# Kernel optimization log

Measured on AMD Instinct MI355X. Metric: run time of the kernel, lower is better.

Reference implementation:

```python
import jax, jax.numpy as jnp
import numpy as np


def setup_inputs() -> dict:
    key = jax.random.key(0)
    k1, k2 = jax.random.split(key)
    N1, N2 = 16384, 16384
    pos1 = jax.random.normal(k1, (N1, 2), dtype=jnp.float32)
    pos2 = jax.random.normal(k2, (N2, 2), dtype=jnp.float32)
    return {"pos1": pos1, "pos2": pos2}


def reference(pos1, pos2):
    # pos1: [N1, 2], pos2: [N2, 2]
    diff = pos1[:, None, :] - pos2[None, :, :]          # [N1, N2, 2]
    dist = jnp.sqrt(jnp.sum(diff * diff, axis=2))       # [N1, N2]
    nearest = jnp.min(dist, axis=1)                     # [N1]
    return jnp.mean(nearest)
```

## Files before the change

kernel.cpp:

```cpp
#include <hip/hip_runtime.h>
#include <math.h>

#define N1 16384
#define N2 16384
#define BLOCK 256
#define PTS 8
#define I_BLOCKS (N1 / (BLOCK * PTS))
#define SLICES 128

__device__ __forceinline__ unsigned int f2key(float f) {
    unsigned int b = __float_as_uint(f);
    return (b & 0x80000000u) ? ~b : (b | 0x80000000u);
}
__device__ __forceinline__ float key2f(unsigned int k) {
    unsigned int b = (k & 0x80000000u) ? (k & 0x7FFFFFFFu) : ~k;
    return __uint_as_float(b);
}

__global__ __launch_bounds__(BLOCK, 4)
void nn_partial(const float2* __restrict__ pos1,
                const float4* __restrict__ pos2,
                unsigned int* __restrict__ keys,
                unsigned int* __restrict__ ticket,
                int slice_f4) {
    const int ib = blockIdx.x;
    const int sl = blockIdx.y;
    const int t  = threadIdx.x;

    if (ib == 0 && sl == 0 && t == 0) *ticket = 0;

    const float4* __restrict__ q = pos2 + (size_t)sl * slice_f4;
    const int i0 = ib * (BLOCK * PTS) + t;

    float x[PTS], y[PTS], m[PTS];
#pragma unroll
    for (int k = 0; k < PTS; ++k) {
        float2 p = pos1[i0 + k * BLOCK];
        x[k] = p.x; y[k] = p.y; m[k] = 3.4e38f;
    }

#pragma unroll 4
    for (int j = 0; j < slice_f4; ++j) {
        float4 qq = q[j];
        float ax = -2.f * qq.x, ay = -2.f * qq.y;
        float az = fmaf(qq.x, qq.x, qq.y * qq.y);
        float bx = -2.f * qq.z, by = -2.f * qq.w;
        float bz = fmaf(qq.z, qq.z, qq.w * qq.w);
#pragma unroll
        for (int k = 0; k < PTS; ++k) {
            m[k] = fminf(m[k], fmaf(x[k], ax, fmaf(y[k], ay, az)));
            m[k] = fminf(m[k], fmaf(x[k], bx, fmaf(y[k], by, bz)));
        }
    }

#pragma unroll
    for (int k = 0; k < PTS; ++k) {
        atomicMin(&keys[i0 + k * BLOCK], f2key(m[k]));
    }
}

__global__ __launch_bounds__(BLOCK)
void nn_finish(const unsigned int* __restrict__ keys,
               const float2* __restrict__ pos1,
               float* __restrict__ blocksums,
               unsigned int* __restrict__ ticket,
               float* __restrict__ out) {
    const int t = threadIdx.x;
    const int i = blockIdx.x * BLOCK + t;

    float g = key2f(keys[i]);
    float2 p = pos1[i];
    float d2 = fmaxf(fmaf(p.x, p.x, p.y * p.y) + g, 0.f);
    float sum = sqrtf(d2);

    for (int off = 32; off > 0; off >>= 1) {
        sum += __shfl_down(sum, off, 64);
    }
    __shared__ float wsum[BLOCK / 64];
    __shared__ int lastflag;
    if ((t & 63) == 0) wsum[t >> 6] = sum;
    __syncthreads();
    if (t == 0) {
        float s = 0.f;
        for (int w = 0; w < BLOCK / 64; ++w) s += wsum[w];
        blocksums[blockIdx.x] = s;
        __threadfence();
        unsigned int old = atomicAdd(ticket, 1u);
        lastflag = (old == gridDim.x - 1) ? 1 : 0;
    }
    __syncthreads();
    if (lastflag && t < 64) {
        volatile float* vb = (volatile float*)blocksums;
        float v = vb[t];
        for (int off = 32; off > 0; off >>= 1) {
            v += __shfl_down(v, off, 64);
        }
        if (t == 0) out[0] = v / (float)N1;
    }
}

extern "C" void kernel_launch(void* const* d_in, const int* in_sizes, int n_in,
                              void* d_out, int out_size, void* d_ws, size_t ws_size,
                              hipStream_t stream) {
    const float2* pos1 = (const float2*)d_in[0];
    const float4* pos2 = (const float4*)d_in[1];
    float* out = (float*)d_out;

    unsigned int* keys = (unsigned int*)d_ws;
    float* blocksums   = (float*)(keys + N1);
    unsigned int* ticket = (unsigned int*)(blocksums + 64);

    const int slice_f4 = (N2 / SLICES) / 2;

    hipMemsetAsync(keys, 0xFF, (size_t)N1 * sizeof(unsigned int), stream);

    dim3 grid1(I_BLOCKS, SLICES);
    nn_partial<<<grid1, BLOCK, 0, stream>>>(pos1, pos2, keys, ticket, slice_f4);
    nn_finish<<<N1 / BLOCK, BLOCK, 0, stream>>>(keys, pos1, blocksums, ticket, out);
}
```

Baseline: 78.07 us.

## Pack FMAs into 2-wide vectors and replace atomicMin with per-slice partials

The inner distance loop now uses 2-wide float vectors so the compiler can emit packed FMA instructions, and the -2 scaling moves onto the pos1 coordinates so it is done once per point instead of per pos2 element. The atomicMin on order-preserving keys and the memset are replaced by plain stores of per-slice minima into an N1×SLICES workspace, which the finish kernel reduces. This removes the atomics and the memset launch, but adds an 8 MB write and read of partials and a 128-iteration serial loop per thread in the finish kernel. The fminf calls stay scalar.

```diff
diff --git a/kernel.cpp b/kernel.cpp
--- a/kernel.cpp
+++ b/kernel.cpp
@@ -5,22 +5,16 @@
 #define N2 16384
 #define BLOCK 256
 #define PTS 8
+#define KK (PTS / 2)
 #define I_BLOCKS (N1 / (BLOCK * PTS))
 #define SLICES 128
 
-__device__ __forceinline__ unsigned int f2key(float f) {
-    unsigned int b = __float_as_uint(f);
-    return (b & 0x80000000u) ? ~b : (b | 0x80000000u);
-}
-__device__ __forceinline__ float key2f(unsigned int k) {
-    unsigned int b = (k & 0x80000000u) ? (k & 0x7FFFFFFFu) : ~k;
-    return __uint_as_float(b);
-}
+typedef float v2f __attribute__((ext_vector_type(2)));
 
 __global__ __launch_bounds__(BLOCK, 4)
 void nn_partial(const float2* __restrict__ pos1,
                 const float4* __restrict__ pos2,
-                unsigned int* __restrict__ keys,
+                float* __restrict__ partials,
                 unsigned int* __restrict__ ticket,
                 int slice_f4) {
     const int ib = blockIdx.x;
@@ -32,35 +26,44 @@
     const float4* __restrict__ q = pos2 + (size_t)sl * slice_f4;
     const int i0 = ib * (BLOCK * PTS) + t;
 
-    float x[PTS], y[PTS], m[PTS];
+    v2f x2[KK], y2[KK], m2[KK];
 #pragma unroll
-    for (int k = 0; k < PTS; ++k) {
-        float2 p = pos1[i0 + k * BLOCK];
-        x[k] = p.x; y[k] = p.y; m[k] = 3.4e38f;
+    for (int k = 0; k < KK; ++k) {
+        float2 p0 = pos1[i0 + (2 * k) * BLOCK];
+        float2 p1 = pos1[i0 + (2 * k + 1) * BLOCK];
+        x2[k] = (v2f){-2.f * p0.x, -2.f * p1.x};
+        y2[k] = (v2f){-2.f * p0.y, -2.f * p1.y};
+        m2[k] = (v2f){3.4e38f, 3.4e38f};
     }
 
 #pragma unroll 4
     for (int j = 0; j < slice_f4; ++j) {
         float4 qq = q[j];
-        float ax = -2.f * qq.x, ay = -2.f * qq.y;
         float az = fmaf(qq.x, qq.x, qq.y * qq.y);
-        float bx = -2.f * qq.z, by = -2.f * qq.w;
         float bz = fmaf(qq.z, qq.z, qq.w * qq.w);
+        v2f AX = {qq.x, qq.x}, AY = {qq.y, qq.y}, AZ = {az, az};
+        v2f BX = {qq.z, qq.z}, BY = {qq.w, qq.w}, BZ = {bz, bz};
 #pragma unroll
-        for (int k = 0; k < PTS; ++k) {
-            m[k] = fminf(m[k], fmaf(x[k], ax, fmaf(y[k], ay, az)));
-            m[k] = fminf(m[k], fmaf(x[k], bx, fmaf(y[k], by, bz)));
+        for (int k = 0; k < KK; ++k) {
+            v2f ta = __builtin_elementwise_fma(
+                x2[k], AX, __builtin_elementwise_fma(y2[k], AY, AZ));
+            v2f tb = __builtin_elementwise_fma(
+                x2[k], BX, __builtin_elementwise_fma(y2[k], BY, BZ));
+            m2[k][0] = fminf(m2[k][0], fminf(ta[0], tb[0]));
+            m2[k][1] = fminf(m2[k][1], fminf(ta[1], tb[1]));
         }
     }
 
+    float* dst = partials + (size_t)sl * N1 + i0;
 #pragma unroll
-    for (int k = 0; k < PTS; ++k) {
-        atomicMin(&keys[i0 + k * BLOCK], f2key(m[k]));
+    for (int k = 0; k < KK; ++k) {
+        dst[(2 * k) * BLOCK]     = m2[k][0];
+        dst[(2 * k + 1) * BLOCK] = m2[k][1];
     }
 }
 
 __global__ __launch_bounds__(BLOCK)
-void nn_finish(const unsigned int* __restrict__ keys,
+void nn_finish(const float* __restrict__ partials,
                const float2* __restrict__ pos1,
                float* __restrict__ blocksums,
                unsigned int* __restrict__ ticket,
@@ -68,7 +71,12 @@
     const int t = threadIdx.x;
     const int i = blockIdx.x * BLOCK + t;
 
-    float g = key2f(keys[i]);
+    float g = 3.4e38f;
+#pragma unroll 16
+    for (int sl = 0; sl < SLICES; ++sl) {
+        g = fminf(g, partials[(size_t)sl * N1 + i]);
+    }
+
     float2 p = pos1[i];
     float d2 = fmaxf(fmaf(p.x, p.x, p.y * p.y) + g, 0.f);
     float sum = sqrtf(d2);
@@ -106,15 +114,13 @@
     const float4* pos2 = (const float4*)d_in[1];
     float* out = (float*)d_out;
 
-    unsigned int* keys = (unsigned int*)d_ws;
-    float* blocksums   = (float*)(keys + N1);
+    float* partials      = (float*)d_ws;
+    float* blocksums     = partials + (size_t)N1 * SLICES;
     unsigned int* ticket = (unsigned int*)(blocksums + 64);
 
     const int slice_f4 = (N2 / SLICES) / 2;
 
-    hipMemsetAsync(keys, 0xFF, (size_t)N1 * sizeof(unsigned int), stream);
-
     dim3 grid1(I_BLOCKS, SLICES);
-    nn_partial<<<grid1, BLOCK, 0, stream>>>(pos1, pos2, keys, ticket, slice_f4);
-    nn_finish<<<N1 / BLOCK, BLOCK, 0, stream>>>(keys, pos1, blocksums, ticket, out);
+    nn_partial<<<grid1, BLOCK, 0, stream>>>(pos1, pos2, partials, ticket, slice_f4);
+    nn_finish<<<N1 / BLOCK, BLOCK, 0, stream>>>(partials, pos1, blocksums, ticket, out);
 }
```

Result: slower. 100.8 us (+29.1%).
